# Kernel optimization log

Measured on AMD Instinct MI355X. Metric: run time of the kernel, lower is better.

## Reference

```python
import jax, jax.numpy as jnp
import numpy as np

NEG_INF = jnp.float32(-(2.0**32) + 1.0)


def squash(z):
    # z: [B, k_max, out_units]
    sq_norm = jnp.sum(jnp.square(z), axis=-1, keepdims=True)
    scale = sq_norm / (1.0 + sq_norm) / jnp.sqrt(sq_norm + 1e-8)
    return scale * z


def setup_inputs() -> dict:
    key = jax.random.key(0)
    k1, k2, k3, k4 = jax.random.split(key, 4)
    B, L, D_IN, D_OUT, K = 1024, 200, 256, 256, 8
    behavior_embeddings = jax.random.normal(k1, (B, L, D_IN), dtype=jnp.float32)
    seq_len = jax.random.randint(k2, (B, 1), 1, L + 1, dtype=jnp.int32)
    routing_logits = jax.random.normal(k3, (1, K, L), dtype=jnp.float32)  # init_std=1.0
    bilinear_mapping_matrix = jax.random.normal(k4, (D_IN, D_OUT), dtype=jnp.float32)
    return {
        "behavior_embeddings": behavior_embeddings,
        "seq_len": seq_len,
        "routing_logits": routing_logits,
        "bilinear_mapping_matrix": bilinear_mapping_matrix,
    }


def reference(behavior_embeddings, seq_len, routing_logits, bilinear_mapping_matrix):
    ITERATION_TIMES = 3
    B, L, _ = behavior_embeddings.shape
    K = routing_logits.shape[1]

    # mask: [B, 1, L] broadcastable to [B, K, L] (same seq_len for every capsule)
    mask = jnp.arange(L)[None, None, :] < seq_len[:, :, None]

    # bilinear map is loop-invariant: [B, L, out_units]
    mapped = jnp.einsum("ble,eo->blo", behavior_embeddings, bilinear_mapping_matrix)

    logits = routing_logits  # [1, K, L]
    interest_capsules = None
    for _ in range(ITERATION_TIMES):
        logits_pad = jnp.where(mask, jnp.broadcast_to(logits, (B, K, L)), NEG_INF)
        weight = jax.nn.softmax(logits_pad, axis=-1)          # [B, K, L]
        Z = jnp.einsum("bkl,blo->bko", weight, mapped)         # [B, K, out]
        interest_capsules = squash(Z)                          # [B, K, out]
        # delta: sum over batch of capsules @ mapped^T -> [1, K, L]
        delta = jnp.einsum("bko,blo->kl", interest_capsules, mapped)[None]
        logits = logits + delta  # emulates assign_add on non-trainable B

    return interest_capsules.reshape(-1, K, interest_capsules.shape[-1])
```

## Files before the change

kernel.cpp:

```cpp
#include <hip/hip_runtime.h>
#include <cstdint>
#include <cstddef>

#define B_    1024
#define L_    200
#define DIN_  256
#define DOUT_ 256
#define K_    8
#define M_    (B_ * L_)

typedef __attribute__((ext_vector_type(8))) short bf16x8;
typedef __attribute__((ext_vector_type(4))) float f32x4;

__device__ __forceinline__ float bf2f(unsigned short u) {
  union { unsigned int i; float f; } w; w.i = ((unsigned int)u) << 16; return w.f;
}
__device__ __forceinline__ unsigned short f2bf(float f) {
  union { float f; unsigned int i; } w; w.f = f;
  unsigned int x = w.i;
  return (unsigned short)((x + 0x7fffu + ((x >> 16) & 1u)) >> 16);
}

__global__ __launch_bounds__(256)
void wt_prep(const float* __restrict__ W, unsigned short* __restrict__ Wh,
             unsigned short* __restrict__ Wm, unsigned short* __restrict__ Wl)
{
  const int k = blockIdx.x;
  const int n = threadIdx.x;
  float x = W[k * DOUT_ + n];
  unsigned short h = f2bf(x);
  float r = x - bf2f(h);
  unsigned short m = f2bf(r);
  float r2 = r - bf2f(m);
  unsigned short l = f2bf(r2);
  const int k0b = k >> 5, quad = (k >> 3) & 3, j = k & 7;
  const int nt = n >> 4, lr = n & 15;
  const size_t idx = ((((size_t)k0b * 16 + nt) * 64) + (quad * 16 + lr)) * 8 + j;
  Wh[idx] = h;
  Wm[idx] = m;
  Wl[idx] = l;
}

__global__ __launch_bounds__(256, 2)
void gemm_mapped(const float* __restrict__ A,
                 const unsigned short* __restrict__ Wh,
                 const unsigned short* __restrict__ Wm,
                 const unsigned short* __restrict__ Wl,
                 float* __restrict__ C)
{
  const int t    = threadIdx.x;
  const int wave = t >> 6;
  const int lane = t & 63;
  const int quad = lane >> 4;
  const int lr   = lane & 15;
  const int m0   = blockIdx.x * 128 + wave * 32;

  f32x4 acc[2][16];
  #pragma unroll
  for (int mt = 0; mt < 2; ++mt)
    #pragma unroll
    for (int nt = 0; nt < 16; ++nt)
      acc[mt][nt] = (f32x4){0.f, 0.f, 0.f, 0.f};

  bf16x8 Bh[4], Bm[4], Bl[4];
  bf16x8 ah[2], am[2], al[2];
  float4 Af[2][2];

#define BLOAD(K0B, NT, S) do { \
    const size_t _off = (((size_t)(K0B) * 16 + (NT)) * 64 + lane) * 8; \
    Bh[S] = *(const bf16x8*)(Wh + _off); \
    Bm[S] = *(const bf16x8*)(Wm + _off); \
    Bl[S] = *(const bf16x8*)(Wl + _off); \
  } while (0)

  const float* ap0 = A + (size_t)(m0 + lr) * DIN_ + quad * 8;
  const float* ap1 = A + (size_t)(m0 + 16 + lr) * DIN_ + quad * 8;

  Af[0][0] = *(const float4*)(ap0);
  Af[0][1] = *(const float4*)(ap0 + 4);
  Af[1][0] = *(const float4*)(ap1);
  Af[1][1] = *(const float4*)(ap1 + 4);
  BLOAD(0, 0, 0); BLOAD(0, 1, 1); BLOAD(0, 2, 2); BLOAD(0, 3, 3);

  for (int k0b = 0; k0b < 8; ++k0b) {
    #pragma unroll
    for (int mt = 0; mt < 2; ++mt) {
      float xs[8] = {Af[mt][0].x, Af[mt][0].y, Af[mt][0].z, Af[mt][0].w,
                     Af[mt][1].x, Af[mt][1].y, Af[mt][1].z, Af[mt][1].w};
      #pragma unroll
      for (int j = 0; j < 8; ++j) {
        unsigned short h = f2bf(xs[j]);
        float r = xs[j] - bf2f(h);
        unsigned short mm = f2bf(r);
        float r2 = r - bf2f(mm);
        unsigned short ll = f2bf(r2);
        ah[mt][j] = (short)h; am[mt][j] = (short)mm; al[mt][j] = (short)ll;
      }
    }
    if (k0b < 7) {
      const int ko = (k0b + 1) * 32;
      Af[0][0] = *(const float4*)(ap0 + ko);
      Af[0][1] = *(const float4*)(ap0 + ko + 4);
      Af[1][0] = *(const float4*)(ap1 + ko);
      Af[1][1] = *(const float4*)(ap1 + ko + 4);
    }

#define GROUP(NT, S) do { \
    f32x4 c0 = acc[0][NT], c1 = acc[1][NT]; \
    c0 = __builtin_amdgcn_mfma_f32_16x16x32_bf16(ah[0], Bh[S], c0, 0, 0, 0); \
    c1 = __builtin_amdgcn_mfma_f32_16x16x32_bf16(ah[1], Bh[S], c1, 0, 0, 0); \
    c0 = __builtin_amdgcn_mfma_f32_16x16x32_bf16(ah[0], Bm[S], c0, 0, 0, 0); \
    c1 = __builtin_amdgcn_mfma_f32_16x16x32_bf16(ah[1], Bm[S], c1, 0, 0, 0); \
    c0 = __builtin_amdgcn_mfma_f32_16x16x32_bf16(am[0], Bh[S], c0, 0, 0, 0); \
    c1 = __builtin_amdgcn_mfma_f32_16x16x32_bf16(am[1], Bh[S], c1, 0, 0, 0); \
    c0 = __builtin_amdgcn_mfma_f32_16x16x32_bf16(ah[0], Bl[S], c0, 0, 0, 0); \
    c1 = __builtin_amdgcn_mfma_f32_16x16x32_bf16(ah[1], Bl[S], c1, 0, 0, 0); \
    c0 = __builtin_amdgcn_mfma_f32_16x16x32_bf16(am[0], Bm[S], c0, 0, 0, 0); \
    c1 = __builtin_amdgcn_mfma_f32_16x16x32_bf16(am[1], Bm[S], c1, 0, 0, 0); \
    c0 = __builtin_amdgcn_mfma_f32_16x16x32_bf16(al[0], Bh[S], c0, 0, 0, 0); \
    c1 = __builtin_amdgcn_mfma_f32_16x16x32_bf16(al[1], Bh[S], c1, 0, 0, 0); \
    acc[0][NT] = c0; acc[1][NT] = c1; \
  } while (0)

    GROUP(0, 0);  BLOAD(k0b, 4, 0);
    GROUP(1, 1);  BLOAD(k0b, 5, 1);
    GROUP(2, 2);  BLOAD(k0b, 6, 2);
    GROUP(3, 3);  BLOAD(k0b, 7, 3);
    GROUP(4, 0);  BLOAD(k0b, 8, 0);
    GROUP(5, 1);  BLOAD(k0b, 9, 1);
    GROUP(6, 2);  BLOAD(k0b, 10, 2);
    GROUP(7, 3);  BLOAD(k0b, 11, 3);
    GROUP(8, 0);  BLOAD(k0b, 12, 0);
    GROUP(9, 1);  BLOAD(k0b, 13, 1);
    GROUP(10, 2); BLOAD(k0b, 14, 2);
    GROUP(11, 3); BLOAD(k0b, 15, 3);
    GROUP(12, 0);
    GROUP(13, 1);
    GROUP(14, 2);
    GROUP(15, 3);
    if (k0b < 7) {
      BLOAD(k0b + 1, 0, 0); BLOAD(k0b + 1, 1, 1);
      BLOAD(k0b + 1, 2, 2); BLOAD(k0b + 1, 3, 3);
    }
#undef GROUP
  }
#undef BLOAD

  #pragma unroll
  for (int mt = 0; mt < 2; ++mt)
    #pragma unroll
    for (int nt = 0; nt < 16; ++nt)
      #pragma unroll
      for (int r = 0; r < 4; ++r) {
        int row = m0 + mt * 16 + quad * 4 + r;
        C[(size_t)row * DOUT_ + nt * 16 + lr] = acc[mt][nt][r];
      }
}

__global__ __launch_bounds__(256)
void z_kernel(const float* __restrict__ mapped, const float* __restrict__ logits,
              const int* __restrict__ seq_len, float* __restrict__ caps)
{
  const int t    = threadIdx.x;
  const int lane = t & 63;
  const int wave = t >> 6;
  const int b    = blockIdx.x * 4 + wave;
  const int len  = seq_len[b];
  __shared__ float w[4][K_][204];

  #pragma unroll
  for (int k = 0; k < K_; ++k) {
    float v[4];
    float mx = -3.4028235e38f;
    #pragma unroll
    for (int i = 0; i < 4; ++i) {
      int l = lane + 64 * i;
      v[i] = (l < len) ? logits[k * L_ + l] : -3.4028235e38f;
      mx = fmaxf(mx, v[i]);
    }
    #pragma unroll
    for (int s = 1; s < 64; s <<= 1) mx = fmaxf(mx, __shfl_xor(mx, s, 64));
    float e[4]; float sum = 0.f;
    #pragma unroll
    for (int i = 0; i < 4; ++i) {
      int l = lane + 64 * i;
      e[i] = (l < len) ? __expf(v[i] - mx) : 0.f;
      sum += e[i];
    }
    #pragma unroll
    for (int s = 1; s < 64; s <<= 1) sum += __shfl_xor(sum, s, 64);
    float inv = 1.f / sum;
    #pragma unroll
    for (int i = 0; i < 4; ++i) {
      int l = lane + 64 * i;
      if (l < 204) w[wave][k][l] = e[i] * inv;
    }
  }

  f32x4 acc[K_];
  #pragma unroll
  for (int k = 0; k < K_; ++k) acc[k] = (f32x4){0.f, 0.f, 0.f, 0.f};
  const float* mp = mapped + (size_t)b * L_ * DOUT_ + lane * 4;
  const int lceil = (len + 3) & ~3;
  for (int l = 0; l < lceil; l += 4) {
    float4 m0 = *(const float4*)(mp + (size_t)(l + 0) * DOUT_);
    float4 m1 = *(const float4*)(mp + (size_t)(l + 1) * DOUT_);
    float4 m2 = *(const float4*)(mp + (size_t)(l + 2) * DOUT_);
    float4 m3 = *(const float4*)(mp + (size_t)(l + 3) * DOUT_);
    #pragma unroll
    for (int k = 0; k < K_; ++k) {
      float4 wv = *(const float4*)&w[wave][k][l];
      f32x4 c = acc[k];
      c.x += wv.x * m0.x + wv.y * m1.x + wv.z * m2.x + wv.w * m3.x;
      c.y += wv.x * m0.y + wv.y * m1.y + wv.z * m2.y + wv.w * m3.y;
      c.z += wv.x * m0.z + wv.y * m1.z + wv.z * m2.z + wv.w * m3.z;
      c.w += wv.x * m0.w + wv.y * m1.w + wv.z * m2.w + wv.w * m3.w;
      acc[k] = c;
    }
  }

  #pragma unroll
  for (int k = 0; k < K_; ++k) {
    float sq = acc[k].x * acc[k].x + acc[k].y * acc[k].y
             + acc[k].z * acc[k].z + acc[k].w * acc[k].w;
    #pragma unroll
    for (int s = 1; s < 64; s <<= 1) sq += __shfl_xor(sq, s, 64);
    float scale = sq / ((1.f + sq) * sqrtf(sq + 1e-8f));
    float4 o;
    o.x = scale * acc[k].x; o.y = scale * acc[k].y;
    o.z = scale * acc[k].z; o.w = scale * acc[k].w;
    *(float4*)&caps[((size_t)b * K_ + k) * DOUT_ + lane * 4] = o;
  }
}

__global__ __launch_bounds__(256)
void delta_kernel(const float* __restrict__ mapped, const float* __restrict__ caps,
                  float* __restrict__ partials)
{
  const int t    = threadIdx.x;
  const int lane = t & 63;
  const int wave = t >> 6;
  const int wid  = blockIdx.x * 4 + wave;
  const int lc   = wid % 25;
  const int bc   = wid / 25;
  const int l0   = lc * 8;
  const int o4   = lane * 4;

  const float* cb = caps   + (size_t)(bc * 16) * (K_ * DOUT_) + o4;
  const float* mb = mapped + ((size_t)(bc * 16) * L_ + l0) * DOUT_ + o4;

  float acc[K_][8];
  #pragma unroll
  for (int k = 0; k < K_; ++k)
    #pragma unroll
    for (int ll = 0; ll < 8; ++ll) acc[k][ll] = 0.f;

  float4 cA[K_], mA[8], cB[K_], mB[8];

#define LOADC(DST, BI) do { \
    const float* _p = cb + (size_t)(BI) * (K_ * DOUT_); \
    _Pragma("unroll") \
    for (int _k = 0; _k < K_; ++_k) DST[_k] = *(const float4*)(_p + _k * DOUT_); \
  } while (0)
#define LOADM(DST, BI) do { \
    const float* _p = mb + (size_t)(BI) * (L_ * DOUT_); \
    _Pragma("unroll") \
    for (int _l = 0; _l < 8; ++_l) DST[_l] = *(const float4*)(_p + _l * DOUT_); \
  } while (0)
#define COMPUTE(CC, MM) do { \
    _Pragma("unroll") \
    for (int _k = 0; _k < K_; ++_k) \
      _Pragma("unroll") \
      for (int _l = 0; _l < 8; ++_l) \
        acc[_k][_l] += CC[_k].x * MM[_l].x + CC[_k].y * MM[_l].y \
                     + CC[_k].z * MM[_l].z + CC[_k].w * MM[_l].w; \
  } while (0)

  LOADC(cA, 0); LOADM(mA, 0);
  for (int i = 0; i < 8; ++i) {
    LOADC(cB, 2 * i + 1); LOADM(mB, 2 * i + 1);
    COMPUTE(cA, mA);
    if (i < 7) { LOADC(cA, 2 * i + 2); LOADM(mA, 2 * i + 2); }
    COMPUTE(cB, mB);
  }
#undef LOADC
#undef LOADM
#undef COMPUTE

  float out = 0.f;
  #pragma unroll
  for (int k = 0; k < K_; ++k)
    #pragma unroll
    for (int ll = 0; ll < 8; ++ll) {
      float v = acc[k][ll];
      v += __shfl_xor(v, 1, 64);
      v += __shfl_xor(v, 2, 64);
      v += __shfl_xor(v, 4, 64);
      v += __shfl_xor(v, 8, 64);
      v += __shfl_xor(v, 16, 64);
      v += __shfl_xor(v, 32, 64);
      if (lane == k * 8 + ll) out = v;
    }
  partials[((size_t)bc * K_ + (lane >> 3)) * L_ + l0 + (lane & 7)] = out;
}

__global__ __launch_bounds__(256)
void init_logits(const float* __restrict__ rlog, float* __restrict__ logits)
{
  int i = blockIdx.x * 256 + threadIdx.x;
  if (i < K_ * L_) logits[i] = rlog[i];
}

__global__ __launch_bounds__(256)
void reduce_kernel(const float* __restrict__ partials, float* __restrict__ logits)
{
  int i = blockIdx.x * 256 + threadIdx.x;
  if (i < K_ * L_) {
    float s = 0.f;
    #pragma unroll 4
    for (int bc = 0; bc < 64; ++bc) s += partials[bc * (K_ * L_) + i];
    logits[i] += s;
  }
}

extern "C" void kernel_launch(void* const* d_in, const int* in_sizes, int n_in,
                              void* d_out, int out_size, void* d_ws, size_t ws_size,
                              hipStream_t stream)
{
  const float* behav = (const float*)d_in[0];
  const int*   slen  = (const int*)d_in[1];
  const float* rlog  = (const float*)d_in[2];
  const float* W     = (const float*)d_in[3];
  float* caps = (float*)d_out;

  char* ws = (char*)d_ws;
  float* logitsW  = (float*)ws;
  float* partials = (float*)(ws + 8192);
  unsigned short* Wh = (unsigned short*)(ws + 458752);
  unsigned short* Wm = (unsigned short*)(ws + 589824);
  unsigned short* Wl = (unsigned short*)(ws + 720896);
  float* mapped   = (float*)(ws + (1 << 20));

  init_logits<<<dim3(7), 256, 0, stream>>>(rlog, logitsW);
  wt_prep<<<dim3(256), 256, 0, stream>>>(W, Wh, Wm, Wl);
  gemm_mapped<<<dim3(1600), 256, 0, stream>>>(behav, Wh, Wm, Wl, mapped);
  for (int it = 0; it < 3; ++it) {
    z_kernel<<<dim3(B_ / 4), 256, 0, stream>>>(mapped, logitsW, slen, caps);
    if (it < 2) {
      delta_kernel<<<dim3(400), 256, 0, stream>>>(mapped, caps, partials);
      reduce_kernel<<<dim3(7), 256, 0, stream>>>(partials, logitsW);
    }
  }
}
```

Before: 635.4 us.

## Split z and delta kernels across more blocks with shared-memory reductions

z_kernel now assigns one batch row per block instead of one per wave. Its four waves split the softmax over capsules and the L loop in strides, then sum their partial accumulators through shared memory before the squash. delta_kernel moves from 400 to 832 blocks, each block tiling 16 batch rows by 16 L positions across four waves and combining the two batch halves in shared memory. The goal is more parallelism and better latency hiding on the memory-bound passes over mapped. The cost is extra syncthreads, shared-memory traffic, and in delta_kernel the loss of the old double-buffered loads plus some wasted lanes past L=200.

Measured after the change: 645.3 us. Within noise of the previous version (+1.6%).

```diff
diff --git a/kernel.cpp b/kernel.cpp
--- a/kernel.cpp
+++ b/kernel.cpp
@@ -161,15 +161,17 @@
 void z_kernel(const float* __restrict__ mapped, const float* __restrict__ logits,
               const int* __restrict__ seq_len, float* __restrict__ caps)
 {
+  const int b    = blockIdx.x;
   const int t    = threadIdx.x;
   const int lane = t & 63;
   const int wave = t >> 6;
-  const int b    = blockIdx.x * 4 + wave;
   const int len  = seq_len[b];
-  __shared__ float w[4][K_][204];
-
-  #pragma unroll
-  for (int k = 0; k < K_; ++k) {
+  __shared__ float w[K_][204];
+  __shared__ float red[4][K_][DOUT_];
+
+  #pragma unroll
+  for (int kk = 0; kk < 2; ++kk) {
+    const int k = wave * 2 + kk;
     float v[4];
     float mx = -3.4028235e38f;
     #pragma unroll
@@ -193,23 +195,24 @@
     #pragma unroll
     for (int i = 0; i < 4; ++i) {
       int l = lane + 64 * i;
-      if (l < 204) w[wave][k][l] = e[i] * inv;
-    }
-  }
+      if (l < 204) w[k][l] = e[i] * inv;
+    }
+  }
+  __syncthreads();
 
   f32x4 acc[K_];
   #pragma unroll
   for (int k = 0; k < K_; ++k) acc[k] = (f32x4){0.f, 0.f, 0.f, 0.f};
   const float* mp = mapped + (size_t)b * L_ * DOUT_ + lane * 4;
   const int lceil = (len + 3) & ~3;
-  for (int l = 0; l < lceil; l += 4) {
+  for (int l = wave * 4; l < lceil; l += 16) {
     float4 m0 = *(const float4*)(mp + (size_t)(l + 0) * DOUT_);
     float4 m1 = *(const float4*)(mp + (size_t)(l + 1) * DOUT_);
     float4 m2 = *(const float4*)(mp + (size_t)(l + 2) * DOUT_);
     float4 m3 = *(const float4*)(mp + (size_t)(l + 3) * DOUT_);
     #pragma unroll
     for (int k = 0; k < K_; ++k) {
-      float4 wv = *(const float4*)&w[wave][k][l];
+      float4 wv = *(const float4*)&w[k][l];
       f32x4 c = acc[k];
       c.x += wv.x * m0.x + wv.y * m1.x + wv.z * m2.x + wv.w * m3.x;
       c.y += wv.x * m0.y + wv.y * m1.y + wv.z * m2.y + wv.w * m3.y;
@@ -218,17 +221,29 @@
       acc[k] = c;
     }
   }
-
-  #pragma unroll
-  for (int k = 0; k < K_; ++k) {
-    float sq = acc[k].x * acc[k].x + acc[k].y * acc[k].y
-             + acc[k].z * acc[k].z + acc[k].w * acc[k].w;
+  #pragma unroll
+  for (int k = 0; k < K_; ++k)
+    *(f32x4*)&red[wave][k][lane * 4] = acc[k];
+  __syncthreads();
+
+  #pragma unroll
+  for (int kk = 0; kk < 2; ++kk) {
+    const int k = wave * 2 + kk;
+    float4 s0 = *(const float4*)&red[0][k][lane * 4];
+    float4 s1 = *(const float4*)&red[1][k][lane * 4];
+    float4 s2 = *(const float4*)&red[2][k][lane * 4];
+    float4 s3 = *(const float4*)&red[3][k][lane * 4];
+    float4 z;
+    z.x = (s0.x + s1.x) + (s2.x + s3.x);
+    z.y = (s0.y + s1.y) + (s2.y + s3.y);
+    z.z = (s0.z + s1.z) + (s2.z + s3.z);
+    z.w = (s0.w + s1.w) + (s2.w + s3.w);
+    float sq = z.x * z.x + z.y * z.y + z.z * z.z + z.w * z.w;
     #pragma unroll
     for (int s = 1; s < 64; s <<= 1) sq += __shfl_xor(sq, s, 64);
     float scale = sq / ((1.f + sq) * sqrtf(sq + 1e-8f));
     float4 o;
-    o.x = scale * acc[k].x; o.y = scale * acc[k].y;
-    o.z = scale * acc[k].z; o.w = scale * acc[k].w;
+    o.x = scale * z.x; o.y = scale * z.y; o.z = scale * z.z; o.w = scale * z.w;
     *(float4*)&caps[((size_t)b * K_ + k) * DOUT_ + lane * 4] = o;
   }
 }
@@ -240,52 +255,39 @@
   const int t    = threadIdx.x;
   const int lane = t & 63;
   const int wave = t >> 6;
-  const int wid  = blockIdx.x * 4 + wave;
-  const int lc   = wid % 25;
-  const int bc   = wid / 25;
-  const int l0   = lc * 8;
+  const int lc   = blockIdx.x % 13;
+  const int bc   = blockIdx.x / 13;
+  const int bsub = (wave >> 1) * 8;
+  const int lsub = (wave & 1) * 8;
+  const int l0   = lc * 16 + lsub;
+  const int b0   = bc * 16 + bsub;
   const int o4   = lane * 4;
 
-  const float* cb = caps   + (size_t)(bc * 16) * (K_ * DOUT_) + o4;
-  const float* mb = mapped + ((size_t)(bc * 16) * L_ + l0) * DOUT_ + o4;
-
   float acc[K_][8];
   #pragma unroll
   for (int k = 0; k < K_; ++k)
     #pragma unroll
     for (int ll = 0; ll < 8; ++ll) acc[k][ll] = 0.f;
 
-  float4 cA[K_], mA[8], cB[K_], mB[8];
-
-#define LOADC(DST, BI) do { \
-    const float* _p = cb + (size_t)(BI) * (K_ * DOUT_); \
-    _Pragma("unroll") \
-    for (int _k = 0; _k < K_; ++_k) DST[_k] = *(const float4*)(_p + _k * DOUT_); \
-  } while (0)
-#define LOADM(DST, BI) do { \
-    const float* _p = mb + (size_t)(BI) * (L_ * DOUT_); \
-    _Pragma("unroll") \
-    for (int _l = 0; _l < 8; ++_l) DST[_l] = *(const float4*)(_p + _l * DOUT_); \
-  } while (0)
-#define COMPUTE(CC, MM) do { \
-    _Pragma("unroll") \
-    for (int _k = 0; _k < K_; ++_k) \
-      _Pragma("unroll") \
-      for (int _l = 0; _l < 8; ++_l) \
-        acc[_k][_l] += CC[_k].x * MM[_l].x + CC[_k].y * MM[_l].y \
-                     + CC[_k].z * MM[_l].z + CC[_k].w * MM[_l].w; \
-  } while (0)
-
-  LOADC(cA, 0); LOADM(mA, 0);
-  for (int i = 0; i < 8; ++i) {
-    LOADC(cB, 2 * i + 1); LOADM(mB, 2 * i + 1);
-    COMPUTE(cA, mA);
-    if (i < 7) { LOADC(cA, 2 * i + 2); LOADM(mA, 2 * i + 2); }
-    COMPUTE(cB, mB);
-  }
-#undef LOADC
-#undef LOADM
-#undef COMPUTE
+  for (int bi = 0; bi < 8; ++bi) {
+    const int b = b0 + bi;
+    const float* cp = caps + (size_t)b * (K_ * DOUT_) + o4;
+    const float* mp = mapped + ((size_t)b * L_ + l0) * DOUT_ + o4;
+    float4 cv[K_], mv[8];
+    #pragma unroll
+    for (int k = 0; k < K_; ++k) cv[k] = *(const float4*)(cp + (size_t)k * DOUT_);
+    #pragma unroll
+    for (int ll = 0; ll < 8; ++ll) {
+      mv[ll] = (l0 + ll < L_) ? *(const float4*)(mp + (size_t)ll * DOUT_)
+                              : make_float4(0.f, 0.f, 0.f, 0.f);
+    }
+    #pragma unroll
+    for (int k = 0; k < K_; ++k)
+      #pragma unroll
+      for (int ll = 0; ll < 8; ++ll)
+        acc[k][ll] += cv[k].x * mv[ll].x + cv[k].y * mv[ll].y
+                    + cv[k].z * mv[ll].z + cv[k].w * mv[ll].w;
+  }
 
   float out = 0.f;
   #pragma unroll
@@ -301,7 +303,16 @@
       v += __shfl_xor(v, 32, 64);
       if (lane == k * 8 + ll) out = v;
     }
-  partials[((size_t)bc * K_ + (lane >> 3)) * L_ + l0 + (lane & 7)] = out;
+  __shared__ float red[4][64];
+  red[wave][lane] = out;
+  __syncthreads();
+  if (wave < 2) {
+    float v = red[wave][lane] + red[wave + 2][lane];
+    const int k  = lane >> 3;
+    const int ll = lane & 7;
+    const int gl = lc * 16 + wave * 8 + ll;
+    if (gl < L_) partials[((size_t)bc * K_ + k) * L_ + gl] = v;
+  }
 }
 
 __global__ __launch_bounds__(256)
@@ -345,9 +356,9 @@
   wt_prep<<<dim3(256), 256, 0, stream>>>(W, Wh, Wm, Wl);
   gemm_mapped<<<dim3(1600), 256, 0, stream>>>(behav, Wh, Wm, Wl, mapped);
   for (int it = 0; it < 3; ++it) {
-    z_kernel<<<dim3(B_ / 4), 256, 0, stream>>>(mapped, logitsW, slen, caps);
+    z_kernel<<<dim3(B_), 256, 0, stream>>>(mapped, logitsW, slen, caps);
     if (it < 2) {
-      delta_kernel<<<dim3(400), 256, 0, stream>>>(mapped, caps, partials);
+      delta_kernel<<<dim3(13 * 64), 256, 0, stream>>>(mapped, caps, partials);
       reduce_kernel<<<dim3(7), 256, 0, stream>>>(partials, logitsW);
     }
   }
```
